# Kernel tuning notes

Measured on AMD Instinct MI355X. Metric: run time of the kernel, lower is better.

## Reference

```python
import jax, jax.numpy as jnp
from jax import lax
import numpy as np

B, N, F_IN, H, K, F_OUT = 8, 4096, 40, 64, 5, 1


def setup_inputs() -> dict:
    key = jax.random.key(0)
    ks = jax.random.split(key, 10)
    x = jax.random.normal(ks[0], (B, N, F_IN), dtype=jnp.float32)
    adjacency_matrix = jax.random.uniform(ks[1], (N, N), dtype=jnp.float32)
    s1 = 1.0 / np.sqrt(F_IN)
    s2 = 1.0 / np.sqrt(H)
    W1 = jax.random.uniform(ks[2], (F_IN, H), minval=-s1, maxval=s1, dtype=jnp.float32)
    b1 = jax.random.uniform(ks[3], (H,), minval=-s1, maxval=s1, dtype=jnp.float32)
    W2 = jax.random.uniform(ks[4], (H, H), minval=-s2, maxval=s2, dtype=jnp.float32)
    b2 = jax.random.uniform(ks[5], (H,), minval=-s2, maxval=s2, dtype=jnp.float32)
    sc = 1.0 / np.sqrt(H * K)
    conv_w = jax.random.uniform(ks[6], (H, H, K), minval=-sc, maxval=sc, dtype=jnp.float32)
    conv_b = jax.random.uniform(ks[7], (H,), minval=-sc, maxval=sc, dtype=jnp.float32)
    fc_w = jax.random.uniform(ks[8], (H, F_OUT), minval=-s2, maxval=s2, dtype=jnp.float32)
    fc_b = jax.random.uniform(ks[9], (F_OUT,), minval=-s2, maxval=s2, dtype=jnp.float32)
    return {"x": x, "adjacency_matrix": adjacency_matrix, "W1": W1, "b1": b1,
            "W2": W2, "b2": b2, "conv_w": conv_w, "conv_b": conv_b,
            "fc_w": fc_w, "fc_b": fc_b}


def reference(x, adjacency_matrix, W1, b1, W2, b2, conv_w, conv_b, fc_w, fc_b):
    # GraphConvolution 1: A @ (x @ W1) + b1  -> [B, N, H]
    h = jnp.einsum('nm,bmh->bnh', adjacency_matrix, x @ W1) + b1
    # GraphConvolution 2: A @ (h @ W2) + b2  -> [B, N, H]
    h = jnp.einsum('nm,bmh->bnh', adjacency_matrix, h @ W2) + b2
    # Temporal Conv1d over node/time axis: channels-first [B, H, N]
    h = jnp.transpose(h, (0, 2, 1))
    h = lax.conv_general_dilated(h, conv_w, window_strides=(1,), padding='VALID',
                                 dimension_numbers=('NCH', 'OIH', 'NCH'))
    h = h + conv_b[None, :, None]  # [B, H, N-K+1]
    h = jnp.mean(h, axis=2)        # mean over length (torch dim=2)
    return h @ fc_w + fc_b         # [B, 1]
```

## Files before the change

### kernel.cpp

```cpp
#include <hip/hip_runtime.h>

#define NN 4096
#define COL4 (NN / 4)
#define BB 8
#define F_IN 40
#define HH 64
#define KW 5
#define LL (NN - KW + 1)
#define RC 32
#define CHUNK (NN / RC)

#define OFF_P1 0
#define OFF_PE (OFF_P1 + RC * NN)
#define OFF_U  (OFF_PE + RC * 8 * NN)
#define OFF_M  (OFF_U + BB * NN)
#define OFF_AB (OFF_M + 9 * F_IN)
#define OFF_G9 (OFF_AB + 9)
#define OFF_RP (OFF_G9 + 9)
#define OFF_SC (OFF_RP + 128)
#define OFF_SD (OFF_SC + 32)
#define OFF_SE (OFF_SD + 8 * 512)

__device__ __forceinline__ int special_row(int s) { return s < 4 ? s : (NN - 8 + s); }
__device__ __forceinline__ void f4add(float4& a, const float4& b) {
    a.x += b.x; a.y += b.y; a.z += b.z; a.w += b.w;
}
__device__ __forceinline__ void f4fma(float4& a, float w, const float4& b) {
    a.x += w * b.x; a.y += w * b.y; a.z += w * b.z; a.w += w * b.w;
}

__global__ __launch_bounds__(256) void k1(const float4* __restrict__ A4,
                                          const float* __restrict__ A,
                                          const float* __restrict__ x,
                                          float4* __restrict__ part1,
                                          float4* __restrict__ partE,
                                          float* __restrict__ rpart,
                                          const float* __restrict__ W1,
                                          const float* __restrict__ b1,
                                          const float* __restrict__ W2,
                                          const float* __restrict__ b2,
                                          const float* __restrict__ cw,
                                          const float* __restrict__ cb,
                                          const float* __restrict__ fw,
                                          const float* __restrict__ fb,
                                          float* __restrict__ Mout,
                                          float* __restrict__ ABout,
                                          float* __restrict__ G9out,
                                          float* __restrict__ u) {
    __shared__ __align__(16) char sm[28928];
    const int tid = threadIdx.x;
    const int tx = tid & 63, ty = tid >> 6;
    if (blockIdx.x < 9) {
        const int v = blockIdx.x;
        float* W2s  = (float*)sm;
        float* W1s  = W2s + 64 * 65;
        float* Xp   = W1s + 40 * 65;
        float* Xs   = Xp + 256;
        float* Ps   = Xs + 64;
        float* bw2s = Ps + 64;
        for (int idx = tid; idx < 64 * 64; idx += 256)
            W2s[(idx >> 6) * 65 + (idx & 63)] = W2[idx];
        for (int idx = tid; idx < 40 * 64; idx += 256)
            W1s[(idx >> 6) * 65 + (idx & 63)] = W1[idx];
        {
            float acc = 0.f;
            for (int oo = 0; oo < 16; ++oo) {
                int o = ty * 16 + oo;
                float f = fw[o];
                const float* cp = cw + ((size_t)o * HH + tx) * KW;
                float w0 = cp[0], w1 = cp[1], w2 = cp[2], w3 = cp[3], w4 = cp[4];
                float coef;
                switch (v) {
                    case 0: coef = w0 + w1 + w2 + w3 + w4; break;
                    case 1: coef = w1 + w2 + w3 + w4; break;
                    case 2: coef = w2 + w3 + w4; break;
                    case 3: coef = w3 + w4; break;
                    case 4: coef = w4; break;
                    case 5: coef = w0; break;
                    case 6: coef = w0 + w1; break;
                    case 7: coef = w0 + w1 + w2; break;
                    default: coef = w0 + w1 + w2 + w3; break;
                }
                acc += f * coef;
            }
            Xp[ty * 64 + tx] = acc;
        }
        __syncthreads();
        if (ty == 0) {
            float s = Xp[tx] + Xp[64 + tx] + Xp[128 + tx] + Xp[192 + tx];
            Xs[tx] = (v == 0 ? 1.f : -1.f) * s / (float)LL;
        }
        __syncthreads();
        if (ty == 0) {
            float s = 0.f;
            #pragma unroll 8
            for (int h = 0; h < 64; ++h) s += b1[h] * W2s[h * 65 + tx];
            bw2s[tx] = s;
        } else if (ty == 1) {
            float s = 0.f;
            #pragma unroll 8
            for (int i = 0; i < 64; ++i) s += Xs[i] * W2s[tx * 65 + i];
            Ps[tx] = s;
        }
        __syncthreads();
        if (tid < F_IN) {
            float s = 0.f;
            #pragma unroll 8
            for (int h = 0; h < 64; ++h) s += Ps[h] * W1s[tid * 65 + h];
            Mout[v * F_IN + tid] = s;
        }
        if (ty == 1) {
            float a = Xs[tx] * bw2s[tx];
            for (int off = 32; off > 0; off >>= 1) a += __shfl_down(a, off);
            if (tx == 0) ABout[v] = a;
        }
        if (ty == 2) {
            float g = Xs[tx] * (v == 0 ? (float)NN * b2[tx] : b2[tx]);
            if (v == 0) g += fw[tx] * cb[tx];
            for (int off = 32; off > 0; off >>= 1) g += __shfl_down(g, off);
            if (tx == 0) G9out[v] = g + (v == 0 ? fb[0] : 0.f);
        }
        return;
    }
    if (blockIdx.x < 73) {
        const int ub = blockIdx.x - 9;
        const int b = ub >> 3, ch = ub & 7;
        float* W2s = (float*)sm;
        float* W1s = W2s + 64 * 65;
        float* Xp  = W1s + 40 * 65;
        float* Xs  = Xp + 256;
        float* Ps  = Xs + 64;
        float* M0s = Ps + 64;
        for (int idx = tid; idx < 64 * 64; idx += 256)
            W2s[(idx >> 6) * 65 + (idx & 63)] = W2[idx];
        for (int idx = tid; idx < 40 * 64; idx += 256)
            W1s[(idx >> 6) * 65 + (idx & 63)] = W1[idx];
        {
            float acc = 0.f;
            for (int oo = 0; oo < 16; ++oo) {
                int o = ty * 16 + oo;
                float f = fw[o];
                const float* cp = cw + ((size_t)o * HH + tx) * KW;
                acc += f * (cp[0] + cp[1] + cp[2] + cp[3] + cp[4]);
            }
            Xp[ty * 64 + tx] = acc;
        }
        __syncthreads();
        if (ty == 0) {
            float s = Xp[tx] + Xp[64 + tx] + Xp[128 + tx] + Xp[192 + tx];
            Xs[tx] = s / (float)LL;
        }
        __syncthreads();
        if (ty == 0) {
            float s = 0.f;
            #pragma unroll 8
            for (int i = 0; i < 64; ++i) s += Xs[i] * W2s[tx * 65 + i];
            Ps[tx] = s;
        }
        __syncthreads();
        if (tid < F_IN) {
            float s = 0.f;
            #pragma unroll 8
            for (int h = 0; h < 64; ++h) s += Ps[h] * W1s[tid * 65 + h];
            M0s[tid] = s;
        }
        __syncthreads();
        const float4* M04 = (const float4*)M0s;
        for (int t = tid; t < 512; t += 256) {
            int col = ch * 512 + t;
            const float4* xr = (const float4*)(x + ((size_t)b * NN + col) * F_IN);
            float s = 0.f;
            #pragma unroll
            for (int q = 0; q < F_IN / 4; ++q) {
                float4 a = xr[q], m = M04[q];
                s += a.x * m.x + a.y * m.y + a.z * m.z + a.w * m.w;
            }
            u[(size_t)b * NN + col] = s;
        }
        return;
    }
    {
        float* wsh = (float*)sm;
        float4 (*red3)[3][64] = (float4 (*)[3][64])(sm + 4096);
        const int sbid = blockIdx.x - 73;
        const int bx = sbid & 15, by = sbid >> 4;
        const int m0 = by * CHUNK;
        for (int idx = tid; idx < 8 * CHUNK; idx += 256) {
            int s = idx >> 7, j = idx & 127;
            wsh[s * CHUNK + j] = A[(size_t)special_row(s) * NN + m0 + j];
        }
        __syncthreads();
        const int c4 = bx * 64 + tx;
        const float4* Ap = A4 + (size_t)(m0 + ty * 32) * COL4 + c4;
        float4 acc[9];
        #pragma unroll
        for (int v = 0; v < 9; ++v) acc[v] = make_float4(0.f, 0.f, 0.f, 0.f);
        #pragma unroll 4
        for (int j = 0; j < 32; ++j) {
            float4 a = Ap[(size_t)j * COL4];
            int jj = ty * 32 + j;
            f4add(acc[0], a);
            #pragma unroll
            for (int s = 0; s < 8; ++s) f4fma(acc[1 + s], wsh[s * CHUNK + jj], a);
        }
        #pragma unroll
        for (int g = 0; g < 3; ++g) {
            #pragma unroll
            for (int vv = 0; vv < 3; ++vv) red3[ty][vv][tx] = acc[g * 3 + vv];
            __syncthreads();
            if (ty == 0) {
                #pragma unroll
                for (int vv = 0; vv < 3; ++vv) {
                    int v = g * 3 + vv;
                    float4 t = red3[0][vv][tx];
                    f4add(t, red3[1][vv][tx]);
                    f4add(t, red3[2][vv][tx]);
                    f4add(t, red3[3][vv][tx]);
                    if (v == 0) part1[(size_t)by * COL4 + c4] = t;
                    else        partE[((size_t)by * 8 + (v - 1)) * COL4 + c4] = t;
                }
            }
            __syncthreads();
        }
        if ((by == 0 || by == 31) && ty == 0) {
            int sbase = (by == 0) ? 0 : 4;
            #pragma unroll
            for (int k = 0; k < 4; ++k) {
                float4 a = A4[(size_t)special_row(sbase + k) * COL4 + c4];
                float v = a.x + a.y + a.z + a.w;
                for (int off = 32; off > 0; off >>= 1) v += __shfl_down(v, off);
                if (tx == 0) rpart[(sbase + k) * 16 + bx] = v;
            }
        }
    }
}

__global__ __launch_bounds__(256) void k2(const float4* __restrict__ A4,
                                          const float* __restrict__ part1f,
                                          const float* __restrict__ partEf,
                                          const float* __restrict__ x,
                                          const float* __restrict__ M,
                                          const float* __restrict__ u,
                                          float* __restrict__ sCpart,
                                          float* __restrict__ spartD,
                                          float* __restrict__ spartE) {
    __shared__ __align__(16) char sm[16384];
    const int tid = threadIdx.x;
    if (blockIdx.x < 512) {
        const int b = blockIdx.x >> 6, pc = blockIdx.x & 63;
        float* xs  = (float*)sm;
        float* wls = xs + 64 * F_IN;
        float* Ms  = wls + 8 * 68;
        float* red = Ms + 320;
        const float4* xsrc4 = (const float4*)(x + ((size_t)b * NN + pc * 64) * F_IN);
        float4* xs4 = (float4*)xs;
        for (int i = tid; i < 64 * F_IN / 4; i += 256) xs4[i] = xsrc4[i];
        for (int i = tid; i < 8 * 16; i += 256) {
            int s = i >> 4, j4 = i & 15;
            float4 t = {0.f, 0.f, 0.f, 0.f};
            #pragma unroll 8
            for (int y = 0; y < RC; ++y)
                f4add(t, ((const float4*)partEf)[((size_t)y * 8 + s) * COL4 + pc * 16 + j4]);
            *(float4*)&wls[s * 68 + j4 * 4] = t;
        }
        for (int i = tid; i < 8 * F_IN; i += 256) Ms[i] = M[F_IN + i];
        __syncthreads();
        float part = 0.f;
        for (int o = tid; o < 8 * F_IN; o += 256) {
            int s = o / F_IN, f = o % F_IN;
            float t = 0.f;
            #pragma unroll 8
            for (int j = 0; j < 64; ++j) t += wls[s * 68 + j] * xs[j * F_IN + f];
            part += Ms[o] * t;
        }
        red[tid] = part;
        __syncthreads();
        for (int off = 128; off > 0; off >>= 1) {
            if (tid < off) red[tid] += red[tid + off];
            __syncthreads();
        }
        if (tid == 0) spartE[(size_t)b * 64 + pc] = red[0];
        return;
    }
    {
        float* cs = (float*)sm;
        float4 (*redd)[64] = (float4 (*)[64])(sm + 512);
        float4* t4s = (float4*)(sm + 4608);
        const int sbid = blockIdx.x - 512;
        const int bx = sbid & 15, by = sbid >> 4;
        const int tx = tid & 63, ty = tid >> 6;
        const int m0 = by * CHUNK;
        if (tid < CHUNK) {
            float s = 0.f;
            #pragma unroll 8
            for (int y = 0; y < RC; ++y) s += part1f[(size_t)y * NN + m0 + tid];
            cs[tid] = s;
        }
        __syncthreads();
        if (bx == 0 && tid < 64) {
            float t = cs[tid] + cs[tid + 64];
            for (int off = 32; off > 0; off >>= 1) t += __shfl_down(t, off);
            if (tid == 0) sCpart[by] = t;
        }
        const int c4 = bx * 64 + tx;
        const float4* Ap = A4 + (size_t)(m0 + ty * 32) * COL4 + c4;
        float4 acc = {0.f, 0.f, 0.f, 0.f};
        #pragma unroll 8
        for (int j = 0; j < 32; ++j) f4fma(acc, cs[ty * 32 + j], Ap[(size_t)j * COL4]);
        redd[ty][tx] = acc;
        __syncthreads();
        if (ty == 0) {
            float4 t = redd[0][tx];
            f4add(t, redd[1][tx]);
            f4add(t, redd[2][tx]);
            f4add(t, redd[3][tx]);
            t4s[tx] = t;
        }
        __syncthreads();
        #pragma unroll
        for (int bb = 0; bb < 2; ++bb) {
            int b = ty * 2 + bb;
            float4 t = t4s[tx];
            float4 uu = ((const float4*)(u + (size_t)b * NN))[c4];
            float val = t.x * uu.x + t.y * uu.y + t.z * uu.z + t.w * uu.w;
            for (int off = 32; off > 0; off >>= 1) val += __shfl_down(val, off);
            if (tx == 0) spartD[(size_t)b * 512 + sbid] = val;
        }
    }
}

__global__ __launch_bounds__(256) void k3(const float* __restrict__ ABp,
                                          const float* __restrict__ G9p,
                                          const float* __restrict__ rpart,
                                          const float* __restrict__ sCpart,
                                          const float* __restrict__ spartD,
                                          const float* __restrict__ spartE,
                                          float* __restrict__ out) {
    __shared__ float red[256];
    __shared__ float c0s;
    const int tid = threadIdx.x;
    float val = 0.f;
    if (tid < 128) val += ABp[1 + (tid >> 4)] * rpart[tid];
    if (tid < 32)  val += ABp[0] * sCpart[tid];
    if (tid < 9)   val += G9p[tid];
    red[tid] = val;
    __syncthreads();
    for (int off = 128; off > 0; off >>= 1) {
        if (tid < off) red[tid] += red[tid + off];
        __syncthreads();
    }
    if (tid == 0) c0s = red[0];
    __syncthreads();
    const int b = tid >> 5, l = tid & 31;
    float s = 0.f;
    #pragma unroll
    for (int k = l; k < 512; k += 32) s += spartD[(size_t)b * 512 + k];
    s += spartE[(size_t)b * 64 + l] + spartE[(size_t)b * 64 + 32 + l];
    for (int off = 16; off > 0; off >>= 1) s += __shfl_down(s, off, 32);
    if (l == 0) out[b] = c0s + s;
}

extern "C" void kernel_launch(void* const* d_in, const int* in_sizes, int n_in,
                              void* d_out, int out_size, void* d_ws, size_t ws_size,
                              hipStream_t stream) {
    const float* x  = (const float*)d_in[0];
    const float* A  = (const float*)d_in[1];
    const float* W1 = (const float*)d_in[2];
    const float* b1 = (const float*)d_in[3];
    const float* W2 = (const float*)d_in[4];
    const float* b2 = (const float*)d_in[5];
    const float* cw = (const float*)d_in[6];
    const float* cb = (const float*)d_in[7];
    const float* fw = (const float*)d_in[8];
    const float* fb = (const float*)d_in[9];
    float* out = (float*)d_out;
    float* ws  = (float*)d_ws;

    float* part1 = ws + OFF_P1;
    float* partE = ws + OFF_PE;
    float* u     = ws + OFF_U;
    float* Mmat  = ws + OFF_M;
    float* ABp   = ws + OFF_AB;
    float* G9p   = ws + OFF_G9;
    float* rpart = ws + OFF_RP;
    float* sCp   = ws + OFF_SC;
    float* spD   = ws + OFF_SD;
    float* spE   = ws + OFF_SE;

    const float4* A4 = (const float4*)A;

    k1<<<dim3(585), 256, 0, stream>>>(A4, A, x, (float4*)part1, (float4*)partE, rpart,
                                      W1, b1, W2, b2, cw, cb, fw, fb, Mmat, ABp, G9p, u);
    k2<<<dim3(1024), 256, 0, stream>>>(A4, part1, partE, x, Mmat, u, sCp, spD, spE);
    k3<<<dim3(1), 256, 0, stream>>>(ABp, G9p, rpart, sCp, spD, spE, out);
}
```

Measured before the change: 44.17 us.

## Restructure k2 E-branch to share reduced weights across batches and coalesce part1 reduction

The E-partial blocks now each handle a 32-node chunk for all 8 batches instead of one batch per 64-node chunk. The partE reduction is split across four thread groups and a combined T = M^T·w matrix is precomputed, so the x contraction becomes a single dot product per batch. This removes the 8x repeated partE reduction and cuts the grid from 512 to 128 blocks for that branch. The D branch stages part1 through shared memory with float4 loads before reducing it, and k3 now reduces 128 E partials per batch instead of 64. Shared memory per block grows to 22.5 KB, which may lower occupancy.

```diff
diff --git a/kernel.cpp b/kernel.cpp
--- a/kernel.cpp
+++ b/kernel.cpp
@@ -244,56 +244,88 @@
                                           float* __restrict__ sCpart,
                                           float* __restrict__ spartD,
                                           float* __restrict__ spartE) {
-    __shared__ __align__(16) char sm[16384];
+    __shared__ __align__(16) char sm[22528];
     const int tid = threadIdx.x;
-    if (blockIdx.x < 512) {
-        const int b = blockIdx.x >> 6, pc = blockIdx.x & 63;
-        float* xs  = (float*)sm;
-        float* wls = xs + 64 * F_IN;
-        float* Ms  = wls + 8 * 68;
-        float* red = Ms + 320;
-        const float4* xsrc4 = (const float4*)(x + ((size_t)b * NN + pc * 64) * F_IN);
-        float4* xs4 = (float4*)xs;
-        for (int i = tid; i < 64 * F_IN / 4; i += 256) xs4[i] = xsrc4[i];
-        for (int i = tid; i < 8 * 16; i += 256) {
-            int s = i >> 4, j4 = i & 15;
+    if (blockIdx.x < 128) {
+        const int pc = blockIdx.x;
+        float4 (*wpart)[8][8] = (float4 (*)[8][8])sm;
+        float* wls = (float*)(sm + 4096);
+        float* Ms  = wls + 8 * 36;
+        float* T   = Ms + 320;
+        float* wred = T + 1280;
+        {
+            int yg = tid >> 6, s = (tid >> 3) & 7, c4 = tid & 7;
             float4 t = {0.f, 0.f, 0.f, 0.f};
-            #pragma unroll 8
-            for (int y = 0; y < RC; ++y)
-                f4add(t, ((const float4*)partEf)[((size_t)y * 8 + s) * COL4 + pc * 16 + j4]);
-            *(float4*)&wls[s * 68 + j4 * 4] = t;
-        }
-        for (int i = tid; i < 8 * F_IN; i += 256) Ms[i] = M[F_IN + i];
-        __syncthreads();
-        float part = 0.f;
-        for (int o = tid; o < 8 * F_IN; o += 256) {
-            int s = o / F_IN, f = o % F_IN;
+            #pragma unroll
+            for (int yy = 0; yy < 8; ++yy) {
+                int y = yg * 8 + yy;
+                f4add(t, ((const float4*)partEf)[((size_t)y * 8 + s) * COL4 + pc * 8 + c4]);
+            }
+            wpart[yg][s][c4] = t;
+        }
+        for (int i = tid; i < 320; i += 256) Ms[i] = M[F_IN + i];
+        __syncthreads();
+        if (tid < 64) {
+            int s = tid >> 3, c4 = tid & 7;
+            float4 t = wpart[0][s][c4];
+            f4add(t, wpart[1][s][c4]);
+            f4add(t, wpart[2][s][c4]);
+            f4add(t, wpart[3][s][c4]);
+            *(float4*)&wls[s * 36 + c4 * 4] = t;
+        }
+        __syncthreads();
+        for (int i = tid; i < 1280; i += 256) {
+            int j = i / 40, f = i % 40;
             float t = 0.f;
-            #pragma unroll 8
-            for (int j = 0; j < 64; ++j) t += wls[s * 68 + j] * xs[j * F_IN + f];
-            part += Ms[o] * t;
-        }
-        red[tid] = part;
-        __syncthreads();
-        for (int off = 128; off > 0; off >>= 1) {
-            if (tid < off) red[tid] += red[tid + off];
-            __syncthreads();
-        }
-        if (tid == 0) spartE[(size_t)b * 64 + pc] = red[0];
+            #pragma unroll
+            for (int s = 0; s < 8; ++s) t += Ms[s * 40 + f] * wls[s * 36 + j];
+            T[i] = t;
+        }
+        __syncthreads();
+        float v[8];
+        const float4* T4 = (const float4*)T;
+        #pragma unroll
+        for (int b = 0; b < 8; ++b) {
+            const float4* xr = (const float4*)(x + ((size_t)b * NN + pc * 32) * F_IN);
+            float acc = 0.f;
+            for (int i = tid; i < 320; i += 256) {
+                float4 a = xr[i], tt = T4[i];
+                acc += a.x * tt.x + a.y * tt.y + a.z * tt.z + a.w * tt.w;
+            }
+            v[b] = acc;
+        }
+        #pragma unroll
+        for (int b = 0; b < 8; ++b)
+            for (int off = 32; off > 0; off >>= 1) v[b] += __shfl_down(v[b], off);
+        if ((tid & 63) == 0) {
+            int wv = tid >> 6;
+            #pragma unroll
+            for (int b = 0; b < 8; ++b) wred[wv * 8 + b] = v[b];
+        }
+        __syncthreads();
+        if (tid < 8)
+            spartE[(size_t)tid * 128 + pc] = wred[tid] + wred[8 + tid] + wred[16 + tid] + wred[24 + tid];
         return;
     }
     {
-        float* cs = (float*)sm;
-        float4 (*redd)[64] = (float4 (*)[64])(sm + 512);
-        float4* t4s = (float4*)(sm + 4608);
-        const int sbid = blockIdx.x - 512;
+        float* csp = (float*)sm;
+        float* cs  = (float*)(sm + 16384);
+        float4 (*redd)[64] = (float4 (*)[64])(sm + 16896);
+        float4* t4s = (float4*)(sm + 20992);
+        const int sbid = blockIdx.x - 128;
         const int bx = sbid & 15, by = sbid >> 4;
         const int tx = tid & 63, ty = tid >> 6;
         const int m0 = by * CHUNK;
-        if (tid < CHUNK) {
-            float s = 0.f;
-            #pragma unroll 8
-            for (int y = 0; y < RC; ++y) s += part1f[(size_t)y * NN + m0 + tid];
+        for (int idx = tid; idx < 1024; idx += 256) {
+            int y = idx >> 5, c4 = idx & 31;
+            float4 vv = ((const float4*)part1f)[(size_t)y * COL4 + (m0 >> 2) + c4];
+            *(float4*)&csp[y * 128 + c4 * 4] = vv;
+        }
+        __syncthreads();
+        if (tid < 128) {
+            float s = 0.f;
+            #pragma unroll 8
+            for (int y = 0; y < 32; ++y) s += csp[y * 128 + tid];
             cs[tid] = s;
         }
         __syncthreads();
@@ -355,7 +387,8 @@
     float s = 0.f;
     #pragma unroll
     for (int k = l; k < 512; k += 32) s += spartD[(size_t)b * 512 + k];
-    s += spartE[(size_t)b * 64 + l] + spartE[(size_t)b * 64 + 32 + l];
+    #pragma unroll
+    for (int k = l; k < 128; k += 32) s += spartE[(size_t)b * 128 + k];
     for (int off = 16; off > 0; off >>= 1) s += __shfl_down(s, off, 32);
     if (l == 0) out[b] = c0s + s;
 }
@@ -391,6 +424,6 @@
 
     k1<<<dim3(585), 256, 0, stream>>>(A4, A, x, (float4*)part1, (float4*)partE, rpart,
                                       W1, b1, W2, b2, cw, cb, fw, fb, Mmat, ABp, G9p, u);
-    k2<<<dim3(1024), 256, 0, stream>>>(A4, part1, partE, x, Mmat, u, sCp, spD, spE);
+    k2<<<dim3(640), 256, 0, stream>>>(A4, part1, partE, x, Mmat, u, sCp, spD, spE);
     k3<<<dim3(1), 256, 0, stream>>>(ABp, G9p, rpart, sCp, spD, spE, out);
 }
```

New measurement: 46.28 us. 4.8% more time.
